# Kernel tuning notes

Measured on AMD Instinct MI355X. Metric: run time of the kernel, lower is better.

Reference implementation:

```python
import jax, jax.numpy as jnp
import numpy as np
from jax import lax

KERNEL = 3
SIGMA = 1.0


def _pdf_gaussian(img):
    # img: [1, 1, H, W]. torch nn.Unfold(k=3, p=1) with zero padding ->
    # patches [1, k*k, H, W] (SAME zero padding), matching torch's [B, L, k*k] after swapaxes.
    patches = lax.conv_general_dilated_patches(
        img, filter_shape=(KERNEL, KERNEL), window_strides=(1, 1), padding='SAME'
    )  # [1, 9, H, W]
    n = KERNEL * KERNEL
    neigh = patches.reshape(1, n, -1).transpose(0, 2, 1)      # [1, HW, 9]
    center = img.reshape(1, -1, 1)                             # [1, HW, 1]
    diff2 = (neigh - center) ** 2
    gauss = jnp.exp(-diff2 / (2.0 * SIGMA * SIGMA))            # [1, HW, 9]
    gauss = gauss / gauss.sum(axis=2, keepdims=True)           # normalize per pixel
    return gauss[0]                                            # [HW, 9]


def setup_inputs() -> dict:
    key = jax.random.key(0)
    k1, k2 = jax.random.split(key)
    H = W = 2048
    pred_real = jax.random.uniform(k1, (1, 1, H, W), dtype=jnp.float32)
    pred_fake = jax.random.uniform(k2, (1, 1, H, W), dtype=jnp.float32)
    return {"pred_real": pred_real, "pred_fake": pred_fake}


def reference(pred_real, pred_fake):
    p = _pdf_gaussian(pred_real)   # [HW, 9]
    q = _pdf_gaussian(pred_fake)   # [HW, 9]
    m = 0.5 * (p + q)
    kl_pq = (p * jnp.log(p / m)).sum(axis=1)   # sum over 9 neighbors
    kl_qp = (q * jnp.log(q / m)).sum(axis=1)
    div = 0.5 * kl_pq + 0.5 * kl_qp            # per-pixel JS divergence
    return 2.0 * div.sum()
```

## Files before the change

### kernel.cpp

```cpp
#include <hip/hip_runtime.h>

static constexpr int H = 2048;
static constexpr int W = 2048;
static constexpr int BLOCK = 256;
static constexpr int NBLOCKS = (H / 2) * (W / (BLOCK * 2));
static constexpr int RBLOCK = 1024;

__device__ __forceinline__ float fexp2(float x){ return __builtin_amdgcn_exp2f(x); }
__device__ __forceinline__ float flog2(float x){ return __builtin_amdgcn_logf(x); }
__device__ __forceinline__ float frcp (float x){ return __builtin_amdgcn_rcpf(x); }

static constexpr float LN2_ = 0.69314718055994531f;
static constexpr float S_   = 0.84932180028801905f;

#define PAIR(e,t, u,v) float e,t; { float d_=(v)-(u); d_*=S_; const float q_=d_*d_; \
                                    e=fexp2(-q_); t=e*q_; }

__device__ __forceinline__ float pixel_term(
    float an0, float an1, float an2, float ca,
    float hAe0, float hAw0, float hAe1, float hAw1,
    float vAe0, float vAw0, float vAe1, float vAw1, float vAe2, float vAw2,
    float bn0, float bn1, float bn2, float cb,
    float hBe0, float hBw0, float hBe1, float hBw1,
    float vBe0, float vBw0, float vBe1, float vBw1, float vBe2, float vBw2)
{
    PAIR(iAe0, iAw0, an0, ca)  PAIR(iAe1, iAw1, an1, ca)  PAIR(iAe2, iAw2, an2, ca)
    PAIR(iBe0, iBw0, bn0, cb)  PAIR(iBe1, iBw1, bn1, cb)  PAIR(iBe2, iBw2, bn2, cb)

    const float Gp  = ((1.f + hAe0) + (hAe1 + vAe0)) + ((vAe1 + vAe2) + (iAe0 + (iAe1 + iAe2)));
    const float Spw = ((hAw0 + hAw1) + (vAw0 + vAw1)) + ((vAw2 + iAw0) + (iAw1 + iAw2));
    const float Gq  = ((1.f + hBe0) + (hBe1 + vBe0)) + ((vBe1 + vBe2) + (iBe0 + (iBe1 + iBe2)));
    const float Sqw = ((hBw0 + hBw1) + (vBw0 + vBw1)) + ((vBw2 + iBw0) + (iBw1 + iBw2));

    const float P  = Gp * Gq;
    const float rP = frcp(P);
    const float ip = rP * Gq;
    const float iq = rP * Gp;
    const float hp = 0.5f * ip, hq = 0.5f * iq;

    float m0 = hp + hq;
    float mllA = m0 * flog2(m0);
    float m1 = fmaf(hAe0, hp, hBe0 * hq);
    float mllB = m1 * flog2(m1);
#define MTA(ea, eb) { const float m_ = fmaf((ea), hp, (eb)*hq); \
                      mllA = fmaf(m_, flog2(m_), mllA); }
#define MTB(ea, eb) { const float m_ = fmaf((ea), hp, (eb)*hq); \
                      mllB = fmaf(m_, flog2(m_), mllB); }
    MTA(hAe1, hBe1)
    MTB(vAe0, vBe0)  MTA(vAe1, vBe1)  MTB(vAe2, vBe2)
    MTA(iAe0, iBe0)  MTB(iAe1, iBe1)  MTA(iAe2, iBe2)
#undef MTA
#undef MTB

    return (fmaf(ip, Spw, iq * Sqw) + flog2(P)) + 2.f * (mllA + mllB);
}

__global__ __launch_bounds__(BLOCK, 4) void jsd_pixel_kernel(
    const float* __restrict__ A, const float* __restrict__ B,
    float* __restrict__ partial)
{
    const int bid   = blockIdx.x;
    const int ytile = bid >> 2;
    const int y0    = ytile << 1;
    const int x0    = ((bid & 3) << 9) + (threadIdx.x << 1);
    const int base  = y0 * W + x0;
    const bool hasL = (x0 > 0);
    const bool hasR = (x0 + 2 < W);

    float a00,a01,a02,a03, a10,a11,a12,a13, a20,a21,a22,a23, a30,a31,a32,a33;
    float b00,b01,b02,b03, b10,b11,b12,b13, b20,b21,b22,b23, b30,b31,b32,b33;

#define LOAD_ROW(p0,p1,p2,p3, ptr, off) \
    { const float2 q_ = *(const float2*)((ptr)+(off)); p1=q_.x; p2=q_.y; \
      p0 = hasL ? (ptr)[(off)-1] : 0.f; p3 = hasR ? (ptr)[(off)+2] : 0.f; }

    LOAD_ROW(a10,a11,a12,a13, A, base)
    LOAD_ROW(a20,a21,a22,a23, A, base + W)
    LOAD_ROW(b10,b11,b12,b13, B, base)
    LOAD_ROW(b20,b21,b22,b23, B, base + W)
    if (y0 > 0) {
        LOAD_ROW(a00,a01,a02,a03, A, base - W)
        LOAD_ROW(b00,b01,b02,b03, B, base - W)
    } else { a00=a01=a02=a03=0.f; b00=b01=b02=b03=0.f; }
    if (y0 + 2 < H) {
        LOAD_ROW(a30,a31,a32,a33, A, base + 2*W)
        LOAD_ROW(b30,b31,b32,b33, B, base + 2*W)
    } else { a30=a31=a32=a33=0.f; b30=b31=b32=b33=0.f; }
#undef LOAD_ROW

    PAIR(hA10,tA10, a10,a11) PAIR(hA11,tA11, a11,a12) PAIR(hA12,tA12, a12,a13)
    PAIR(hA20,tA20, a20,a21) PAIR(hA21,tA21, a21,a22) PAIR(hA22,tA22, a22,a23)
    PAIR(hB10,tB10, b10,b11) PAIR(hB11,tB11, b11,b12) PAIR(hB12,tB12, b12,b13)
    PAIR(hB20,tB20, b20,b21) PAIR(hB21,tB21, b21,b22) PAIR(hB22,tB22, b22,b23)
    PAIR(vA10,wA10, a11,a20) PAIR(vA11,wA11, a11,a21) PAIR(vA12,wA12, a11,a22)
    PAIR(vA21,wA21, a12,a21) PAIR(vA22,wA22, a12,a22) PAIR(vA23,wA23, a12,a23)
    PAIR(vA01,wA01, a10,a21) PAIR(vA32,wA32, a13,a22)
    PAIR(vB10,wB10, b11,b20) PAIR(vB11,wB11, b11,b21) PAIR(vB12,wB12, b11,b22)
    PAIR(vB21,wB21, b12,b21) PAIR(vB22,wB22, b12,b22) PAIR(vB23,wB23, b12,b23)
    PAIR(vB01,wB01, b10,b21) PAIR(vB32,wB32, b13,b22)

    const float t0 = pixel_term(a00,a01,a02, a11, hA10,tA10, hA11,tA11,
                                vA10,wA10, vA11,wA11, vA12,wA12,
                                b00,b01,b02, b11, hB10,tB10, hB11,tB11,
                                vB10,wB10, vB11,wB11, vB12,wB12);
    const float t1 = pixel_term(a01,a02,a03, a12, hA11,tA11, hA12,tA12,
                                vA21,wA21, vA22,wA22, vA23,wA23,
                                b01,b02,b03, b12, hB11,tB11, hB12,tB12,
                                vB21,wB21, vB22,wB22, vB23,wB23);
    const float t2 = pixel_term(a30,a31,a32, a21, hA20,tA20, hA21,tA21,
                                vA01,wA01, vA11,wA11, vA21,wA21,
                                b30,b31,b32, b21, hB20,tB20, hB21,tB21,
                                vB01,wB01, vB11,wB11, vB21,wB21);
    const float t3 = pixel_term(a31,a32,a33, a22, hA21,tA21, hA22,tA22,
                                vA12,wA12, vA22,wA22, vA32,wA32,
                                b31,b32,b33, b22, hB21,tB21, hB22,tB22,
                                vB12,wB12, vB22,wB22, vB32,wB32);
    float pacc = (t0 + t1) + (t2 + t3);

    #pragma unroll
    for (int off = 32; off > 0; off >>= 1)
        pacc += __shfl_down(pacc, off, 64);

    __shared__ float wsum[BLOCK / 64];
    const int lane = threadIdx.x & 63;
    const int wid  = threadIdx.x >> 6;
    if (lane == 0) wsum[wid] = pacc;
    __syncthreads();
    if (threadIdx.x == 0)
        partial[blockIdx.x] = (wsum[0] + wsum[1]) + (wsum[2] + wsum[3]);
}

__global__ __launch_bounds__(RBLOCK) void jsd_final_reduce(
    const float* __restrict__ partial, float* __restrict__ out)
{
    float s = 0.f;
    #pragma unroll
    for (int i = 0; i < NBLOCKS / RBLOCK; ++i)
        s += partial[i * RBLOCK + threadIdx.x];

    #pragma unroll
    for (int off = 32; off > 0; off >>= 1)
        s += __shfl_down(s, off, 64);

    __shared__ float wsum[RBLOCK / 64];
    const int lane = threadIdx.x & 63;
    const int wid  = threadIdx.x >> 6;
    if (lane == 0) wsum[wid] = s;
    __syncthreads();
    if (threadIdx.x == 0) {
        float t = 0.f;
        #pragma unroll
        for (int i = 0; i < RBLOCK / 64; ++i) t += wsum[i];
        out[0] = -LN2_ * t;
    }
}

extern "C" void kernel_launch(void* const* d_in, const int* in_sizes, int n_in,
                              void* d_out, int out_size, void* d_ws, size_t ws_size,
                              hipStream_t stream) {
    const float* A = (const float*)d_in[0];
    const float* B = (const float*)d_in[1];
    float* out = (float*)d_out;
    float* partial = (float*)d_ws;

    jsd_pixel_kernel<<<NBLOCKS, BLOCK, 0, stream>>>(A, B, partial);
    jsd_final_reduce<<<1, RBLOCK, 0, stream>>>(partial, out);
}
```

Measured before the change: 27.17 us.

## Process 2x4 pixel tiles per thread to share more pair exponentials

Each thread now covers a 2x4 pixel tile instead of 2x2, loading rows with float4 plus halo elements. Symmetric neighbour-pair Gaussian terms (horizontal, vertical, diagonal) are computed once and shared across adjacent pixels, which cuts the exp2 count per pixel and the redundant halo loads. The block count halves and the launch-bounds occupancy hint drops from 4 to 3 blocks per CU to allow more registers. The trade-off is higher register pressure and fewer blocks to hide latency.

```diff
diff --git a/kernel.cpp b/kernel.cpp
--- a/kernel.cpp
+++ b/kernel.cpp
@@ -3,7 +3,7 @@
 static constexpr int H = 2048;
 static constexpr int W = 2048;
 static constexpr int BLOCK = 256;
-static constexpr int NBLOCKS = (H / 2) * (W / (BLOCK * 2));
+static constexpr int NBLOCKS = (H / 2) * (W / (BLOCK * 4));
 static constexpr int RBLOCK = 1024;
 
 __device__ __forceinline__ float fexp2(float x){ return __builtin_amdgcn_exp2f(x); }
@@ -16,21 +16,16 @@
 #define PAIR(e,t, u,v) float e,t; { float d_=(v)-(u); d_*=S_; const float q_=d_*d_; \
                                     e=fexp2(-q_); t=e*q_; }
 
-__device__ __forceinline__ float pixel_term(
-    float an0, float an1, float an2, float ca,
-    float hAe0, float hAw0, float hAe1, float hAw1,
-    float vAe0, float vAw0, float vAe1, float vAw1, float vAe2, float vAw2,
-    float bn0, float bn1, float bn2, float cb,
-    float hBe0, float hBw0, float hBe1, float hBw1,
-    float vBe0, float vBw0, float vBe1, float vBw1, float vBe2, float vBw2)
+__device__ __forceinline__ float pixel_term8(
+    float a0,float u0, float a1,float u1, float a2,float u2, float a3,float u3,
+    float a4,float u4, float a5,float u5, float a6,float u6, float a7,float u7,
+    float b0,float v0, float b1,float v1, float b2,float v2, float b3,float v3,
+    float b4,float v4, float b5,float v5, float b6,float v6, float b7,float v7)
 {
-    PAIR(iAe0, iAw0, an0, ca)  PAIR(iAe1, iAw1, an1, ca)  PAIR(iAe2, iAw2, an2, ca)
-    PAIR(iBe0, iBw0, bn0, cb)  PAIR(iBe1, iBw1, bn1, cb)  PAIR(iBe2, iBw2, bn2, cb)
-
-    const float Gp  = ((1.f + hAe0) + (hAe1 + vAe0)) + ((vAe1 + vAe2) + (iAe0 + (iAe1 + iAe2)));
-    const float Spw = ((hAw0 + hAw1) + (vAw0 + vAw1)) + ((vAw2 + iAw0) + (iAw1 + iAw2));
-    const float Gq  = ((1.f + hBe0) + (hBe1 + vBe0)) + ((vBe1 + vBe2) + (iBe0 + (iBe1 + iBe2)));
-    const float Sqw = ((hBw0 + hBw1) + (vBw0 + vBw1)) + ((vBw2 + iBw0) + (iBw1 + iBw2));
+    const float Gp  = ((1.f + a0) + (a1 + a2)) + ((a3 + a4) + (a5 + (a6 + a7)));
+    const float Spw = ((u0 + u1) + (u2 + u3)) + ((u4 + u5) + (u6 + u7));
+    const float Gq  = ((1.f + b0) + (b1 + b2)) + ((b3 + b4) + (b5 + (b6 + b7)));
+    const float Sqw = ((v0 + v1) + (v2 + v3)) + ((v4 + v5) + (v6 + v7));
 
     const float P  = Gp * Gq;
     const float rP = frcp(P);
@@ -40,82 +35,139 @@
 
     float m0 = hp + hq;
     float mllA = m0 * flog2(m0);
-    float m1 = fmaf(hAe0, hp, hBe0 * hq);
+    float m1 = fmaf(a0, hp, b0 * hq);
     float mllB = m1 * flog2(m1);
 #define MTA(ea, eb) { const float m_ = fmaf((ea), hp, (eb)*hq); \
                       mllA = fmaf(m_, flog2(m_), mllA); }
 #define MTB(ea, eb) { const float m_ = fmaf((ea), hp, (eb)*hq); \
                       mllB = fmaf(m_, flog2(m_), mllB); }
-    MTA(hAe1, hBe1)
-    MTB(vAe0, vBe0)  MTA(vAe1, vBe1)  MTB(vAe2, vBe2)
-    MTA(iAe0, iBe0)  MTB(iAe1, iBe1)  MTA(iAe2, iBe2)
+    MTA(a1,b1) MTB(a2,b2) MTA(a3,b3) MTB(a4,b4) MTA(a5,b5) MTB(a6,b6) MTA(a7,b7)
 #undef MTA
 #undef MTB
 
     return (fmaf(ip, Spw, iq * Sqw) + flog2(P)) + 2.f * (mllA + mllB);
 }
 
-__global__ __launch_bounds__(BLOCK, 4) void jsd_pixel_kernel(
+__global__ __launch_bounds__(BLOCK, 3) void jsd_pixel_kernel(
     const float* __restrict__ A, const float* __restrict__ B,
     float* __restrict__ partial)
 {
-    const int bid   = blockIdx.x;
-    const int ytile = bid >> 2;
-    const int y0    = ytile << 1;
-    const int x0    = ((bid & 3) << 9) + (threadIdx.x << 1);
-    const int base  = y0 * W + x0;
-    const bool hasL = (x0 > 0);
-    const bool hasR = (x0 + 2 < W);
-
-    float a00,a01,a02,a03, a10,a11,a12,a13, a20,a21,a22,a23, a30,a31,a32,a33;
-    float b00,b01,b02,b03, b10,b11,b12,b13, b20,b21,b22,b23, b30,b31,b32,b33;
-
-#define LOAD_ROW(p0,p1,p2,p3, ptr, off) \
-    { const float2 q_ = *(const float2*)((ptr)+(off)); p1=q_.x; p2=q_.y; \
-      p0 = hasL ? (ptr)[(off)-1] : 0.f; p3 = hasR ? (ptr)[(off)+2] : 0.f; }
-
-    LOAD_ROW(a10,a11,a12,a13, A, base)
-    LOAD_ROW(a20,a21,a22,a23, A, base + W)
-    LOAD_ROW(b10,b11,b12,b13, B, base)
-    LOAD_ROW(b20,b21,b22,b23, B, base + W)
+    const int bid  = blockIdx.x;
+    const int y0   = (bid >> 1) << 1;
+    const int col0 = ((bid & 1) << 10) + (threadIdx.x << 2);
+    const int base = y0 * W + col0;
+    const bool hasL = (col0 > 0);
+    const bool hasR = (col0 + 4 < W);
+
+    float a00,a01,a02,a03,a04,a05, a10,a11,a12,a13,a14,a15;
+    float a20,a21,a22,a23,a24,a25, a30,a31,a32,a33,a34,a35;
+    float b00,b01,b02,b03,b04,b05, b10,b11,b12,b13,b14,b15;
+    float b20,b21,b22,b23,b24,b25, b30,b31,b32,b33,b34,b35;
+
+#define LOAD_ROW6(p0,p1,p2,p3,p4,p5, ptr, off) \
+    { const float4 q_ = *(const float4*)((ptr)+(off)); \
+      p1=q_.x; p2=q_.y; p3=q_.z; p4=q_.w; \
+      p0 = hasL ? (ptr)[(off)-1] : 0.f; p5 = hasR ? (ptr)[(off)+4] : 0.f; }
+
+    LOAD_ROW6(a10,a11,a12,a13,a14,a15, A, base)
+    LOAD_ROW6(a20,a21,a22,a23,a24,a25, A, base + W)
+    LOAD_ROW6(b10,b11,b12,b13,b14,b15, B, base)
+    LOAD_ROW6(b20,b21,b22,b23,b24,b25, B, base + W)
     if (y0 > 0) {
-        LOAD_ROW(a00,a01,a02,a03, A, base - W)
-        LOAD_ROW(b00,b01,b02,b03, B, base - W)
-    } else { a00=a01=a02=a03=0.f; b00=b01=b02=b03=0.f; }
+        LOAD_ROW6(a00,a01,a02,a03,a04,a05, A, base - W)
+        LOAD_ROW6(b00,b01,b02,b03,b04,b05, B, base - W)
+    } else { a00=a01=a02=a03=a04=a05=0.f; b00=b01=b02=b03=b04=b05=0.f; }
     if (y0 + 2 < H) {
-        LOAD_ROW(a30,a31,a32,a33, A, base + 2*W)
-        LOAD_ROW(b30,b31,b32,b33, B, base + 2*W)
-    } else { a30=a31=a32=a33=0.f; b30=b31=b32=b33=0.f; }
-#undef LOAD_ROW
-
-    PAIR(hA10,tA10, a10,a11) PAIR(hA11,tA11, a11,a12) PAIR(hA12,tA12, a12,a13)
-    PAIR(hA20,tA20, a20,a21) PAIR(hA21,tA21, a21,a22) PAIR(hA22,tA22, a22,a23)
-    PAIR(hB10,tB10, b10,b11) PAIR(hB11,tB11, b11,b12) PAIR(hB12,tB12, b12,b13)
-    PAIR(hB20,tB20, b20,b21) PAIR(hB21,tB21, b21,b22) PAIR(hB22,tB22, b22,b23)
-    PAIR(vA10,wA10, a11,a20) PAIR(vA11,wA11, a11,a21) PAIR(vA12,wA12, a11,a22)
-    PAIR(vA21,wA21, a12,a21) PAIR(vA22,wA22, a12,a22) PAIR(vA23,wA23, a12,a23)
-    PAIR(vA01,wA01, a10,a21) PAIR(vA32,wA32, a13,a22)
-    PAIR(vB10,wB10, b11,b20) PAIR(vB11,wB11, b11,b21) PAIR(vB12,wB12, b11,b22)
-    PAIR(vB21,wB21, b12,b21) PAIR(vB22,wB22, b12,b22) PAIR(vB23,wB23, b12,b23)
-    PAIR(vB01,wB01, b10,b21) PAIR(vB32,wB32, b13,b22)
-
-    const float t0 = pixel_term(a00,a01,a02, a11, hA10,tA10, hA11,tA11,
-                                vA10,wA10, vA11,wA11, vA12,wA12,
-                                b00,b01,b02, b11, hB10,tB10, hB11,tB11,
-                                vB10,wB10, vB11,wB11, vB12,wB12);
-    const float t1 = pixel_term(a01,a02,a03, a12, hA11,tA11, hA12,tA12,
-                                vA21,wA21, vA22,wA22, vA23,wA23,
-                                b01,b02,b03, b12, hB11,tB11, hB12,tB12,
-                                vB21,wB21, vB22,wB22, vB23,wB23);
-    const float t2 = pixel_term(a30,a31,a32, a21, hA20,tA20, hA21,tA21,
-                                vA01,wA01, vA11,wA11, vA21,wA21,
-                                b30,b31,b32, b21, hB20,tB20, hB21,tB21,
-                                vB01,wB01, vB11,wB11, vB21,wB21);
-    const float t3 = pixel_term(a31,a32,a33, a22, hA21,tA21, hA22,tA22,
-                                vA12,wA12, vA22,wA22, vA32,wA32,
-                                b31,b32,b33, b22, hB21,tB21, hB22,tB22,
-                                vB12,wB12, vB22,wB22, vB32,wB32);
-    float pacc = (t0 + t1) + (t2 + t3);
+        LOAD_ROW6(a30,a31,a32,a33,a34,a35, A, base + 2*W)
+        LOAD_ROW6(b30,b31,b32,b33,b34,b35, B, base + 2*W)
+    } else { a30=a31=a32=a33=a34=a35=0.f; b30=b31=b32=b33=b34=b35=0.f; }
+#undef LOAD_ROW6
+
+    PAIR(hA1a,sA1a, a11,a12) PAIR(hA1b,sA1b, a12,a13) PAIR(hA1c,sA1c, a13,a14)
+    PAIR(hA2a,sA2a, a21,a22) PAIR(hA2b,sA2b, a22,a23) PAIR(hA2c,sA2c, a23,a24)
+    PAIR(vA1,xA1, a11,a21) PAIR(vA2,xA2, a12,a22) PAIR(vA3,xA3, a13,a23) PAIR(vA4,xA4, a14,a24)
+    PAIR(pA1,yA1, a11,a22) PAIR(pA2,yA2, a12,a23) PAIR(pA3,yA3, a13,a24)
+    PAIR(qA1,zA1, a12,a21) PAIR(qA2,zA2, a13,a22) PAIR(qA3,zA3, a14,a23)
+    PAIR(hB1a,sB1a, b11,b12) PAIR(hB1b,sB1b, b12,b13) PAIR(hB1c,sB1c, b13,b14)
+    PAIR(hB2a,sB2a, b21,b22) PAIR(hB2b,sB2b, b22,b23) PAIR(hB2c,sB2c, b23,b24)
+    PAIR(vB1,xB1, b11,b21) PAIR(vB2,xB2, b12,b22) PAIR(vB3,xB3, b13,b23) PAIR(vB4,xB4, b14,b24)
+    PAIR(pB1,yB1, b11,b22) PAIR(pB2,yB2, b12,b23) PAIR(pB3,yB3, b13,b24)
+    PAIR(qB1,zB1, b12,b21) PAIR(qB2,zB2, b13,b22) PAIR(qB3,zB3, b14,b23)
+
+    float pacc = 0.f;
+
+    {
+      PAIR(ua0,wa0, a00,a11) PAIR(ua1,wa1, a01,a11) PAIR(ua2,wa2, a02,a11)
+      PAIR(ua3,wa3, a10,a11) PAIR(ua4,wa4, a11,a20)
+      PAIR(ub0,wb0, b00,b11) PAIR(ub1,wb1, b01,b11) PAIR(ub2,wb2, b02,b11)
+      PAIR(ub3,wb3, b10,b11) PAIR(ub4,wb4, b11,b20)
+      pacc += pixel_term8(ua0,wa0, ua1,wa1, ua2,wa2, ua3,wa3, ua4,wa4,
+                          hA1a,sA1a, vA1,xA1, pA1,yA1,
+                          ub0,wb0, ub1,wb1, ub2,wb2, ub3,wb3, ub4,wb4,
+                          hB1a,sB1a, vB1,xB1, pB1,yB1);
+    }
+    {
+      PAIR(ua0,wa0, a01,a12) PAIR(ua1,wa1, a02,a12) PAIR(ua2,wa2, a03,a12)
+      PAIR(ub0,wb0, b01,b12) PAIR(ub1,wb1, b02,b12) PAIR(ub2,wb2, b03,b12)
+      pacc += pixel_term8(ua0,wa0, ua1,wa1, ua2,wa2, hA1a,sA1a, hA1b,sA1b,
+                          qA1,zA1, vA2,xA2, pA2,yA2,
+                          ub0,wb0, ub1,wb1, ub2,wb2, hB1a,sB1a, hB1b,sB1b,
+                          qB1,zB1, vB2,xB2, pB2,yB2);
+    }
+    {
+      PAIR(ua0,wa0, a02,a13) PAIR(ua1,wa1, a03,a13) PAIR(ua2,wa2, a04,a13)
+      PAIR(ub0,wb0, b02,b13) PAIR(ub1,wb1, b03,b13) PAIR(ub2,wb2, b04,b13)
+      pacc += pixel_term8(ua0,wa0, ua1,wa1, ua2,wa2, hA1b,sA1b, hA1c,sA1c,
+                          qA2,zA2, vA3,xA3, pA3,yA3,
+                          ub0,wb0, ub1,wb1, ub2,wb2, hB1b,sB1b, hB1c,sB1c,
+                          qB2,zB2, vB3,xB3, pB3,yB3);
+    }
+    {
+      PAIR(ua0,wa0, a03,a14) PAIR(ua1,wa1, a04,a14) PAIR(ua2,wa2, a05,a14)
+      PAIR(ua3,wa3, a14,a15) PAIR(ua4,wa4, a14,a25)
+      PAIR(ub0,wb0, b03,b14) PAIR(ub1,wb1, b04,b14) PAIR(ub2,wb2, b05,b14)
+      PAIR(ub3,wb3, b14,b15) PAIR(ub4,wb4, b14,b25)
+      pacc += pixel_term8(ua0,wa0, ua1,wa1, ua2,wa2, ua3,wa3, ua4,wa4,
+                          hA1c,sA1c, qA3,zA3, vA4,xA4,
+                          ub0,wb0, ub1,wb1, ub2,wb2, ub3,wb3, ub4,wb4,
+                          hB1c,sB1c, qB3,zB3, vB4,xB4);
+    }
+    {
+      PAIR(ua0,wa0, a30,a21) PAIR(ua1,wa1, a31,a21) PAIR(ua2,wa2, a32,a21)
+      PAIR(ua3,wa3, a20,a21) PAIR(ua4,wa4, a10,a21)
+      PAIR(ub0,wb0, b30,b21) PAIR(ub1,wb1, b31,b21) PAIR(ub2,wb2, b32,b21)
+      PAIR(ub3,wb3, b20,b21) PAIR(ub4,wb4, b10,b21)
+      pacc += pixel_term8(ua0,wa0, ua1,wa1, ua2,wa2, ua3,wa3, ua4,wa4,
+                          hA2a,sA2a, vA1,xA1, qA1,zA1,
+                          ub0,wb0, ub1,wb1, ub2,wb2, ub3,wb3, ub4,wb4,
+                          hB2a,sB2a, vB1,xB1, qB1,zB1);
+    }
+    {
+      PAIR(ua0,wa0, a31,a22) PAIR(ua1,wa1, a32,a22) PAIR(ua2,wa2, a33,a22)
+      PAIR(ub0,wb0, b31,b22) PAIR(ub1,wb1, b32,b22) PAIR(ub2,wb2, b33,b22)
+      pacc += pixel_term8(ua0,wa0, ua1,wa1, ua2,wa2, hA2a,sA2a, hA2b,sA2b,
+                          pA1,yA1, vA2,xA2, qA2,zA2,
+                          ub0,wb0, ub1,wb1, ub2,wb2, hB2a,sB2a, hB2b,sB2b,
+                          pB1,yB1, vB2,xB2, qB2,zB2);
+    }
+    {
+      PAIR(ua0,wa0, a32,a23) PAIR(ua1,wa1, a33,a23) PAIR(ua2,wa2, a34,a23)
+      PAIR(ub0,wb0, b32,b23) PAIR(ub1,wb1, b33,b23) PAIR(ub2,wb2, b34,b23)
+      pacc += pixel_term8(ua0,wa0, ua1,wa1, ua2,wa2, hA2b,sA2b, hA2c,sA2c,
+                          pA2,yA2, vA3,xA3, qA3,zA3,
+                          ub0,wb0, ub1,wb1, ub2,wb2, hB2b,sB2b, hB2c,sB2c,
+                          pB2,yB2, vB3,xB3, qB3,zB3);
+    }
+    {
+      PAIR(ua0,wa0, a33,a24) PAIR(ua1,wa1, a34,a24) PAIR(ua2,wa2, a35,a24)
+      PAIR(ua3,wa3, a24,a25) PAIR(ua4,wa4, a15,a24)
+      PAIR(ub0,wb0, b33,b24) PAIR(ub1,wb1, b34,b24) PAIR(ub2,wb2, b35,b24)
+      PAIR(ub3,wb3, b24,b25) PAIR(ub4,wb4, b15,b24)
+      pacc += pixel_term8(ua0,wa0, ua1,wa1, ua2,wa2, ua3,wa3, ua4,wa4,
+                          hA2c,sA2c, pA3,yA3, vA4,xA4,
+                          ub0,wb0, ub1,wb1, ub2,wb2, ub3,wb3, ub4,wb4,
+                          hB2c,sB2c, pB3,yB3, vB4,xB4);
+    }
 
     #pragma unroll
     for (int off = 32; off > 0; off >>= 1)
```

Measured after the change: 27.06 us. Within noise of the previous version (-0.4%).
